# Optimization experiments

Hardware: AMD Instinct MI355X
Metric: run time of the kernel (lower is better)

Reference implementation:

```python
import jax, jax.numpy as jnp
import numpy as np

EPS = 1e-5

def _conv1x1(x, w, b):
    # x: [B, Cin, L], w: [Cout, Cin], b: [Cout]
    return jnp.einsum('oc,bcl->bol', w, x) + b[None, :, None]

def _bn(x, g, b):
    # BatchNorm1d in training mode: batch stats over (B, L), biased variance
    m = jnp.mean(x, axis=(0, 2), keepdims=True)
    v = jnp.var(x, axis=(0, 2), keepdims=True)
    return g[None, :, None] * (x - m) * jax.lax.rsqrt(v + EPS) + b[None, :, None]

def setup_inputs() -> dict:
    key = jax.random.key(0)
    ks = jax.random.split(key, 16)
    B, H, L, K = 32, 32, 32768, 7
    rel, im, out = H // 16, H // 8, H // 4          # 2, 4, 8
    cat = (1 + K) * rel                              # 16
    w = lambda k, shape: jax.random.normal(k, shape, jnp.float32) * 0.1
    return {
        'x': jax.random.normal(ks[0], (B, H, L), jnp.float32),
        'w_phi': w(ks[1], (rel, H)),  'b_phi': w(ks[2], (rel,)),
        'w_psi': w(ks[3], (rel, H)),  'b_psi': w(ks[4], (rel,)),
        'w_beta': w(ks[5], (out, H)), 'b_beta': w(ks[6], (out,)),
        'w_cw1': w(ks[7], (im, cat)), 'b_cw1': w(ks[8], (im,)),
        'w_cw2': w(ks[9], (out, im)), 'b_cw2': w(ks[10], (out,)),
        'w_out': w(ks[11], (H, out)), 'b_out': w(ks[12], (H,)),
        'g_cat': jnp.ones((cat,), jnp.float32),  'be_cat': jnp.zeros((cat,), jnp.float32),
        'g_im': jnp.ones((im,), jnp.float32),    'be_im': jnp.zeros((im,), jnp.float32),
        'g_aggr': jnp.ones((out,), jnp.float32), 'be_aggr': jnp.zeros((out,), jnp.float32),
        'g_hid': jnp.ones((H,), jnp.float32),    'be_hid': jnp.zeros((H,), jnp.float32),
        'kernel_size': 7,
    }

def reference(x, w_phi, b_phi, w_psi, b_psi, w_beta, b_beta,
              w_cw1, b_cw1, w_cw2, b_cw2, w_out, b_out,
              g_cat, be_cat, g_im, be_im, g_aggr, be_aggr, g_hid, be_hid,
              kernel_size):
    B, H, L = x.shape
    phi = _conv1x1(x, w_phi, b_phi)                       # [B, rel, L]
    psi = _conv1x1(x, w_psi, b_psi)                       # [B, rel, L]
    p = kernel_size // 2
    psi_pad = jnp.pad(psi, ((0, 0), (0, 0), (p, p)))
    # F.unfold with kernel (k,1): channel index = c*k + j -> stack kernel axis after channel
    psi_unf = jnp.stack([psi_pad[:, :, j:j + L] for j in range(kernel_size)], axis=2)
    psi_unf = psi_unf.reshape(B, psi.shape[1] * kernel_size, L)   # [B, rel*k, L]
    h = jnp.concatenate([phi, psi_unf], axis=1)           # [B, (1+k)*rel, L]
    h = jax.nn.relu(_bn(h, g_cat, be_cat))
    h = _conv1x1(h, w_cw1, b_cw1)
    h = jax.nn.relu(_bn(h, g_im, be_im))
    weight = _conv1x1(h, w_cw2, b_cw2)                    # [B, out, L]
    beta = _conv1x1(x, w_beta, b_beta)                    # [B, out, L]
    aggr = jax.nn.relu(_bn(weight * beta, g_aggr, be_aggr))
    y = x + _conv1x1(aggr, w_out, b_out)
    return jax.nn.relu(_bn(y, g_hid, be_hid))
```

## Files before the change

### kernel.cpp

```cpp
#include <hip/hip_runtime.h>
#include <math.h>

#define Bn 32
#define Hc 32
#define Ln 32768
#define RELC 2
#define IMC 4
#define OC 8
#define CATC 16
#define KS 7
#define NPOS (Bn*Ln)
#define TPB 256
#define VPT 4
#define PPB (TPB*VPT)
#define TILES (Ln/PPB)
#define NBLK (Bn*TILES)
#define NSLOT 16
#define SSTR 128
#define PCH (RELC*PPB)
#define BCH (OC*PPB)
#define XCH (Hc*PPB)

#define iS_PHI  0
#define iSS_PHI 2
#define iS_PSI  4
#define iSS_PSI 6
#define iS_T    8
#define iSS_T   12
#define iS_AP   16
#define iSS_AP  24
#define iS_Y    32
#define iSS_Y   64
#define bPF  0
#define bPFS 6
#define bQL  12
#define bQLS 18
#define NBST 24

#define FMA4(A,S,V) { A.x=fmaf((S),(V).x,A.x); A.y=fmaf((S),(V).y,A.y); A.z=fmaf((S),(V).z,A.z); A.w=fmaf((S),(V).w,A.w); }

__device__ inline float4 affrelu(float4 v, float a, float d){
    float4 r;
    r.x=fmaxf(fmaf(a,v.x,d),0.f); r.y=fmaxf(fmaf(a,v.y,d),0.f);
    r.z=fmaxf(fmaf(a,v.z,d),0.f); r.w=fmaxf(fmaf(a,v.w,d),0.f);
    return r;
}
__device__ inline double wredd(double v){
    #pragma unroll
    for (int o=32;o>0;o>>=1) v += __shfl_down(v,o,64);
    return v;
}
__device__ inline float wredf(float v){
    #pragma unroll
    for (int o=32;o>0;o>>=1) v += __shfl_down(v,o,64);
    return v;
}
__device__ inline void atomAddD(double* p, double v){ unsafeAtomicAdd(p, v); }

__device__ inline unsigned short f2b(float f){
    unsigned int u = __float_as_uint(f);
    u += 0x7FFFu + ((u>>16)&1u);
    return (unsigned short)(u>>16);
}
__device__ inline float b2f(unsigned short h){ return __uint_as_float(((unsigned int)h)<<16); }
__device__ inline ushort4 pack4r(float4 v, float4* r){
    ushort4 h;
    h.x=f2b(v.x); h.y=f2b(v.y); h.z=f2b(v.z); h.w=f2b(v.w);
    r->x=b2f(h.x); r->y=b2f(h.y); r->z=b2f(h.z); r->w=b2f(h.w);
    return h;
}
__device__ inline ushort4 pack4(float4 v){
    ushort4 h;
    h.x=f2b(v.x); h.y=f2b(v.y); h.z=f2b(v.z); h.w=f2b(v.w);
    return h;
}
__device__ inline float4 unpack4(ushort4 h){
    return make_float4(b2f(h.x),b2f(h.y),b2f(h.z),b2f(h.w));
}
typedef unsigned short us8 __attribute__((ext_vector_type(8)));
typedef float f4nt __attribute__((ext_vector_type(4)));
__device__ inline void ntstore4(float* p, float4 v){
    union { float4 a; f4nt b; } u; u.a = v;
    __builtin_nontemporal_store(u.b, (f4nt*)p);
}

template<int NCH>
__device__ void affines(const double* __restrict__ stats, const double* __restrict__ bstats,
                        const float* g_cat, const float* be_cat,
                        const float* g_im,  const float* be_im,
                        const float* g_ag,  const float* be_ag,
                        const float* g_hid, const float* be_hid,
                        double (*redS)[16], double (*redQ)[16],
                        double* bstL, float* aAll, float* dAll, int tid)
{
    if (tid < NBST) bstL[tid] = bstats[tid];
    for (int p = tid; p < NCH*16; p += TPB){
        int ch = p >> 4, s = p & 15;
        int si, qi;
        if (ch < 2)       { si = iS_PHI+ch;           qi = iSS_PHI+ch; }
        else if (ch < 16) { int cp=(ch-2)/KS;         si = iS_PSI+cp;  qi = iSS_PSI+cp; }
        else if (ch < 20) { int i=ch-16;              si = iS_T+i;     qi = iSS_T+i; }
        else if (ch < 28) { int o=ch-20;              si = iS_AP+o;    qi = iSS_AP+o; }
        else              { int h=ch-28;              si = iS_Y+h;     qi = iSS_Y+h; }
        redS[ch][s] = stats[(size_t)s*SSTR + si];
        redQ[ch][s] = stats[(size_t)s*SSTR + qi];
    }
    __syncthreads();
    if (tid < NCH){
        double S=0, SS=0;
        #pragma unroll
        for (int s=0;s<16;++s){ S += redS[tid][s]; SS += redQ[tid][s]; }
        float g, be;
        if (tid < 16){
            if (tid >= 2){
                int cp=(tid-2)/KS, j=(tid-2)%KS, d=j-KS/2;
                if (d>0) for (int i=0;i<d;++i)   { S-=bstL[bPF+cp*3+i]; SS-=bstL[bPFS+cp*3+i]; }
                if (d<0) for (int i=3+d;i<3;++i) { S-=bstL[bQL+cp*3+i]; SS-=bstL[bQLS+cp*3+i]; }
            }
            g=g_cat[tid]; be=be_cat[tid];
        } else if (tid < 20){ g=g_im[tid-16]; be=be_im[tid-16]; }
        else if (tid < 28){ g=g_ag[tid-20]; be=be_ag[tid-20]; }
        else { g=g_hid[tid-28]; be=be_hid[tid-28]; }
        const double N=(double)NPOS;
        double m=S/N, v=SS/N-m*m, inv=1.0/sqrt(v+1e-5);
        aAll[tid]=(float)(g*inv);
        dAll[tid]=be-(float)(m*inv*g);
    }
}

__global__ void __launch_bounds__(TPB) k0(const float* __restrict__ x, unsigned short* __restrict__ xC)
{
    const int r = blockIdx.x;
    const int b = r >> 5, h = r & 31;
    const float* src = x + (size_t)r*Ln;
    unsigned short* dstBase = xC + (size_t)b*TILES*XCH + (size_t)h*PPB + threadIdx.x*4;
    const float* s4 = src + threadIdx.x*4;
    #pragma unroll 4
    for (int t = 0; t < TILES; ++t){
        float4 v = *(const float4*)(s4 + (size_t)t*PPB);
        *(ushort4*)(dstBase + (size_t)t*XCH) = pack4(v);
    }
}

__global__ void __launch_bounds__(TPB) k1c(
    const unsigned short* __restrict__ xC,
    const float* __restrict__ w_phi, const float* __restrict__ b_phi,
    const float* __restrict__ w_psi, const float* __restrict__ b_psi,
    const float* __restrict__ w_beta,const float* __restrict__ b_beta,
    unsigned short* __restrict__ phiC, unsigned short* __restrict__ psiC,
    unsigned short* __restrict__ betaC,
    double* __restrict__ stats, double* __restrict__ bstats)
{
    __shared__ __align__(16) float wl[Hc*12 + 12];
    __shared__ double rbuf[4][8];
    const int tid = threadIdx.x;
    for (int i = tid; i < Hc*12; i += TPB) {
        int h = i/12, j = i%12;
        float v;
        if (j < 2)      v = w_phi[j*Hc + h];
        else if (j < 4) v = w_psi[(j-2)*Hc + h];
        else            v = w_beta[(j-4)*Hc + h];
        wl[h*12 + j] = v;
    }
    if (tid < 12)
        wl[Hc*12+tid] = (tid<2) ? b_phi[tid] : (tid<4) ? b_psi[tid-2] : b_beta[tid-4];
    __syncthreads();

    const int cidx = blockIdx.x;
    const int tile = cidx % TILES;
    const int li   = tid*VPT;
    double* st = stats + (size_t)(cidx & (NSLOT-1))*SSTR;

    float4 acc[12];
    #pragma unroll
    for (int j=0;j<12;++j){ float bb = wl[Hc*12+j]; acc[j]=make_float4(bb,bb,bb,bb); }

    const unsigned short* xb = xC + (size_t)cidx*XCH + li;
    #pragma unroll
    for (int g=0; g<4; ++g){
        ushort4 xv[8];
        #pragma unroll
        for (int j=0;j<8;++j) xv[j] = *(const ushort4*)(xb + (size_t)(g*8+j)*PPB);
        #pragma unroll
        for (int j=0;j<8;++j){
            const int h = g*8+j;
            const float4 x4 = unpack4(xv[j]);
            const float4 w0 = *(const float4*)(&wl[h*12+0]);
            const float4 w1 = *(const float4*)(&wl[h*12+4]);
            const float4 w2 = *(const float4*)(&wl[h*12+8]);
            FMA4(acc[0],w0.x,x4); FMA4(acc[1],w0.y,x4); FMA4(acc[2],w0.z,x4); FMA4(acc[3],w0.w,x4);
            FMA4(acc[4],w1.x,x4); FMA4(acc[5],w1.y,x4); FMA4(acc[6],w1.z,x4); FMA4(acc[7],w1.w,x4);
            FMA4(acc[8],w2.x,x4); FMA4(acc[9],w2.y,x4); FMA4(acc[10],w2.z,x4); FMA4(acc[11],w2.w,x4);
        }
    }
    float4 rphi[2], rpsi[2];
    #pragma unroll
    for (int c=0;c<RELC;++c){
        ushort4 hp = pack4r(acc[c], &rphi[c]);
        *(ushort4*)(phiC + (size_t)cidx*PCH + c*PPB + li) = hp;
        ushort4 hq = pack4r(acc[2+c], &rpsi[c]);
        *(ushort4*)(psiC + (size_t)cidx*PCH + c*PPB + li) = hq;
    }
    #pragma unroll
    for (int o=0;o<OC;++o)
        *(ushort4*)(betaC + (size_t)cidx*BCH + o*PPB + li) = pack4(acc[4+o]);

    double vals[8];
    #pragma unroll
    for (int c=0;c<2;++c){
        float4 v = rphi[c];
        vals[c]   = (double)v.x+v.y+v.z+v.w;
        vals[2+c] = (double)v.x*v.x+(double)v.y*v.y+(double)v.z*v.z+(double)v.w*v.w;
        float4 u = rpsi[c];
        vals[4+c] = (double)u.x+u.y+u.z+u.w;
        vals[6+c] = (double)u.x*u.x+(double)u.y*u.y+(double)u.z*u.z+(double)u.w*u.w;
    }
    if (tile==0 || tile==TILES-1) {
        #pragma unroll
        for (int c=0;c<2;++c){
            const float pv[4] = {rpsi[c].x, rpsi[c].y, rpsi[c].z, rpsi[c].w};
            #pragma unroll
            for (int e=0;e<4;++e){
                int le = tile*PPB + li + e;
                if (le < 3) {
                    atomAddD(&bstats[bPF +c*3+le], (double)pv[e]);
                    atomAddD(&bstats[bPFS+c*3+le], (double)pv[e]*pv[e]);
                }
                if (le >= Ln-3) {
                    int i = le-(Ln-3);
                    atomAddD(&bstats[bQL +c*3+i], (double)pv[e]);
                    atomAddD(&bstats[bQLS+c*3+i], (double)pv[e]*pv[e]);
                }
            }
        }
    }
    const int lane=tid&63, wid=tid>>6;
    #pragma unroll
    for (int i=0;i<8;++i){ double r=wredd(vals[i]); if(lane==0) rbuf[wid][i]=r; }
    __syncthreads();
    if (tid<8) atomAddD(&st[iS_PHI+tid], rbuf[0][tid]+rbuf[1][tid]+rbuf[2][tid]+rbuf[3][tid]);
}

#define STAGE_PSI_V(psiT)                                                                  \
    {                                                                                      \
        int c_ = tid >> 7, k_ = tid & 127;                                                 \
        us8 v_ = *(const us8*)(psiC + (size_t)cidx*PCH + c_*PPB + 8*k_);                   \
        _Pragma("unroll")                                                                  \
        for (int j_=0;j_<8;++j_) psiT[c_][3+8*k_+j_] = b2f(v_[j_]);                        \
        if (tid < 6){ int cc=tid/3, ii=tid%3;                                              \
            psiT[cc][ii] = (tile>0) ? b2f(psiC[(size_t)(cidx-1)*PCH + cc*PPB + 1021+ii]) : 0.f; }\
        else if (tid < 12){ int kk=tid-6, cc=kk/3, ii=kk%3;                                \
            psiT[cc][1027+ii] = (tile<TILES-1) ? b2f(psiC[(size_t)(cidx+1)*PCH + cc*PPB + ii]) : 0.f; } \
    }

#define COMPUTE_T(tacc,aCat,dCat,w1s,b1s,psiT)                                             \
    _Pragma("unroll")                                                                      \
    for (int o=0;o<IMC;++o){ float bb=b1s[o]; tacc[o]=make_float4(bb,bb,bb,bb); }          \
    _Pragma("unroll")                                                                      \
    for (int c=0;c<RELC;++c){                                                              \
        float4 pv = unpack4(*(const ushort4*)(phiC + (size_t)cidx*PCH + c*PPB + li));      \
        float4 hv = affrelu(pv, aCat[c], dCat[c]);                                         \
        _Pragma("unroll")                                                                  \
        for (int o=0;o<IMC;++o) FMA4(tacc[o], w1s[o*CATC+c], hv);                          \
    }                                                                                      \
    _Pragma("unroll")                                                                      \
    for (int c=0;c<RELC;++c){                                                              \
        float4 A  = *(const float4*)&psiT[c][li];                                          \
        float4 Bv = *(const float4*)&psiT[c][li+4];                                        \
        float4 Cv = *(const float4*)&psiT[c][li+8];                                        \
        float pr[12] = {A.x,A.y,A.z,A.w, Bv.x,Bv.y,Bv.z,Bv.w, Cv.x,Cv.y,Cv.z,Cv.w};        \
        _Pragma("unroll")                                                                  \
        for (int j=0;j<KS;++j){                                                            \
            int ch = 2 + c*KS + j;                                                         \
            float a=aCat[ch], d=dCat[ch];                                                  \
            float4 hv;                                                                     \
            hv.x=fmaxf(fmaf(a,pr[j+0],d),0.f);                                             \
            hv.y=fmaxf(fmaf(a,pr[j+1],d),0.f);                                             \
            hv.z=fmaxf(fmaf(a,pr[j+2],d),0.f);                                             \
            hv.w=fmaxf(fmaf(a,pr[j+3],d),0.f);                                             \
            _Pragma("unroll")                                                              \
            for (int o=0;o<IMC;++o) FMA4(tacc[o], w1s[o*CATC+ch], hv);                     \
        }                                                                                  \
    }

#define COMPUTE_AG(ag,tacc,aIm,dIm,aAg,dAg,w2s,b2s)                                        \
    {                                                                                      \
        float4 h2[IMC];                                                                    \
        _Pragma("unroll")                                                                  \
        for (int i=0;i<IMC;++i) h2[i]=affrelu(tacc[i],aIm[i],dIm[i]);                      \
        _Pragma("unroll")                                                                  \
        for (int o=0;o<OC;++o){                                                            \
            float bb=b2s[o];                                                               \
            float4 w=make_float4(bb,bb,bb,bb);                                             \
            _Pragma("unroll")                                                              \
            for (int i=0;i<IMC;++i) FMA4(w,w2s[o*IMC+i],h2[i]);                            \
            float4 bv = unpack4(*(const ushort4*)(betaC + (size_t)cidx*BCH + o*PPB + li)); \
            float4 av; av.x=w.x*bv.x; av.y=w.y*bv.y; av.z=w.z*bv.z; av.w=w.w*bv.w;         \
            ag[o]=affrelu(av, aAg[o], dAg[o]);                                             \
        }                                                                                  \
    }

__global__ void __launch_bounds__(TPB) k3t(
    const unsigned short* __restrict__ phiC, const unsigned short* __restrict__ psiC,
    const float* __restrict__ w_cw1, const float* __restrict__ b_cw1,
    const float* __restrict__ g_cat, const float* __restrict__ be_cat,
    double* __restrict__ stats, const double* __restrict__ bstats)
{
    __shared__ float w1s[IMC*CATC], b1s[IMC];
    __shared__ __align__(16) float psiT[2][1032];
    __shared__ double rbuf[4][8];
    __shared__ double redS[16][16], redQ[16][16];
    __shared__ double bstL[NBST];
    __shared__ float aAll[16], dAll[16];
    const int tid = threadIdx.x;
    const int cidx = blockIdx.x;
    const int tile = cidx % TILES;
    const int li   = tid*VPT;
    double* st = stats + (size_t)(cidx & (NSLOT-1))*SSTR;

    if (tid < IMC*CATC) w1s[tid] = w_cw1[tid];
    if (tid < IMC)      b1s[tid] = b_cw1[tid];
    STAGE_PSI_V(psiT)
    affines<16>(stats,bstats, g_cat,be_cat, 0,0, 0,0, 0,0, redS,redQ,bstL,aAll,dAll, tid);
    __syncthreads();

    float4 tacc[IMC];
    COMPUTE_T(tacc,aAll,dAll,w1s,b1s,psiT)

    double vals[8];
    #pragma unroll
    for (int o=0;o<IMC;++o){
        float4 v = tacc[o];
        vals[o]   = (double)v.x+v.y+v.z+v.w;
        vals[4+o] = (double)v.x*v.x+(double)v.y*v.y+(double)v.z*v.z+(double)v.w*v.w;
    }
    const int lane=tid&63, wid=tid>>6;
    #pragma unroll
    for (int i=0;i<8;++i){ double r=wredd(vals[i]); if(lane==0) rbuf[wid][i]=r; }
    __syncthreads();
    if (tid<8) atomAddD(&st[iS_T+tid], rbuf[0][tid]+rbuf[1][tid]+rbuf[2][tid]+rbuf[3][tid]);
}

__global__ void __launch_bounds__(TPB) k5a(
    const unsigned short* __restrict__ phiC, const unsigned short* __restrict__ psiC,
    const unsigned short* __restrict__ betaC,
    const float* __restrict__ w_cw1, const float* __restrict__ b_cw1,
    const float* __restrict__ w_cw2, const float* __restrict__ b_cw2,
    const float* __restrict__ g_cat, const float* __restrict__ be_cat,
    const float* __restrict__ g_im,  const float* __restrict__ be_im,
    double* __restrict__ stats, const double* __restrict__ bstats)
{
    __shared__ float w1s[IMC*CATC], b1s[IMC], w2s[OC*IMC], b2s[OC];
    __shared__ __align__(16) float psiT[2][1032];
    __shared__ double rbuf[4][16];
    __shared__ double redS[20][16], redQ[20][16];
    __shared__ double bstL[NBST];
    __shared__ float aAll[20], dAll[20];
    const int tid = threadIdx.x;
    const int cidx = blockIdx.x;
    const int tile = cidx % TILES;
    const int li   = tid*VPT;
    double* st = stats + (size_t)(cidx & (NSLOT-1))*SSTR;

    if (tid < IMC*CATC) w1s[tid] = w_cw1[tid];
    if (tid < IMC)      b1s[tid] = b_cw1[tid];
    if (tid>=64 && tid<64+OC*IMC) w2s[tid-64]=w_cw2[tid-64];
    if (tid>=96 && tid<96+OC)     b2s[tid-96]=b_cw2[tid-96];
    STAGE_PSI_V(psiT)
    affines<20>(stats,bstats, g_cat,be_cat, g_im,be_im, 0,0, 0,0, redS,redQ,bstL,aAll,dAll, tid);
    __syncthreads();

    float4 tacc[IMC];
    COMPUTE_T(tacc,aAll,dAll,w1s,b1s,psiT)

    double vals[16];
    {
        float4 h2[IMC];
        #pragma unroll
        for (int i=0;i<IMC;++i) h2[i]=affrelu(tacc[i],aAll[16+i],dAll[16+i]);
        #pragma unroll
        for (int o=0;o<OC;++o){
            float bb=b2s[o];
            float4 w=make_float4(bb,bb,bb,bb);
            #pragma unroll
            for (int i=0;i<IMC;++i) FMA4(w,w2s[o*IMC+i],h2[i]);
            float4 bv = unpack4(*(const ushort4*)(betaC + (size_t)cidx*BCH + o*PPB + li));
            float4 av; av.x=w.x*bv.x; av.y=w.y*bv.y; av.z=w.z*bv.z; av.w=w.w*bv.w;
            vals[o]   = (double)av.x+av.y+av.z+av.w;
            vals[8+o] = (double)av.x*av.x+(double)av.y*av.y+(double)av.z*av.z+(double)av.w*av.w;
        }
    }
    const int lane=tid&63, wid=tid>>6;
    #pragma unroll
    for (int i=0;i<16;++i){ double r=wredd(vals[i]); if(lane==0) rbuf[wid][i]=r; }
    __syncthreads();
    if (tid<16) atomAddD(&st[iS_AP+tid], rbuf[0][tid]+rbuf[1][tid]+rbuf[2][tid]+rbuf[3][tid]);
}

__global__ void __launch_bounds__(TPB) k7y(
    const unsigned short* __restrict__ xC,
    const unsigned short* __restrict__ phiC, const unsigned short* __restrict__ psiC,
    const unsigned short* __restrict__ betaC, unsigned short* __restrict__ agC,
    const float* __restrict__ w_cw1, const float* __restrict__ b_cw1,
    const float* __restrict__ w_cw2, const float* __restrict__ b_cw2,
    const float* __restrict__ w_out, const float* __restrict__ b_out,
    const float* __restrict__ g_cat, const float* __restrict__ be_cat,
    const float* __restrict__ g_im,  const float* __restrict__ be_im,
    const float* __restrict__ g_ag,  const float* __restrict__ be_ag,
    double* __restrict__ stats, const double* __restrict__ bstats)
{
    __shared__ float w1s[IMC*CATC], b1s[IMC], w2s[OC*IMC], b2s[OC];
    __shared__ __align__(16) float wos[Hc*OC];
    __shared__ float bos[Hc];
    __shared__ __align__(16) float psiT[2][1032];
    __shared__ float fredS[Hc][4], fredQ[Hc][4];
    __shared__ double redS[28][16], redQ[28][16];
    __shared__ double bstL[NBST];
    __shared__ float aAll[28], dAll[28];
    const int tid = threadIdx.x;
    const int cidx = blockIdx.x;
    const int tile = cidx % TILES;
    const int li   = tid*VPT;
    double* st = stats + (size_t)(cidx & (NSLOT-1))*SSTR;

    if (tid < IMC*CATC) w1s[tid] = w_cw1[tid];
    if (tid < IMC)      b1s[tid] = b_cw1[tid];
    if (tid>=64 && tid<64+OC*IMC) w2s[tid-64]=w_cw2[tid-64];
    if (tid>=96 && tid<96+OC)     b2s[tid-96]=b_cw2[tid-96];
    wos[tid] = w_out[tid];
    if (tid>=128 && tid<128+Hc) bos[tid-128]=b_out[tid-128];
    STAGE_PSI_V(psiT)
    affines<28>(stats,bstats, g_cat,be_cat, g_im,be_im, g_ag,be_ag, 0,0,
                redS,redQ,bstL,aAll,dAll, tid);
    __syncthreads();

    float4 tacc[IMC];
    COMPUTE_T(tacc,aAll,dAll,w1s,b1s,psiT)
    float4 ag[OC];
    COMPUTE_AG(ag,tacc,(aAll+16),(dAll+16),(aAll+20),(dAll+20),w2s,b2s)
    #pragma unroll
    for (int o=0;o<OC;++o){
        ushort4 hh = pack4r(ag[o], &ag[o]);
        *(ushort4*)(agC + (size_t)cidx*BCH + o*PPB + li) = hh;
    }

    const int lane=tid&63, wid=tid>>6;
    const unsigned short* xb = xC + (size_t)cidx*XCH + li;
    #pragma unroll
    for (int g=0; g<4; ++g){
        ushort4 xv[8];
        #pragma unroll
        for (int j=0;j<8;++j) xv[j] = *(const ushort4*)(xb + (size_t)(g*8+j)*PPB);
        #pragma unroll
        for (int j=0;j<8;++j){
            const int h = g*8+j;
            float4 y = unpack4(xv[j]);
            float bb=bos[h]; y.x+=bb; y.y+=bb; y.z+=bb; y.w+=bb;
            #pragma unroll
            for (int o=0;o<OC;++o) FMA4(y, wos[h*OC+o], ag[o]);
            float fs=y.x+y.y+y.z+y.w;
            float fq=y.x*y.x+y.y*y.y+y.z*y.z+y.w*y.w;
            fs=wredf(fs); fq=wredf(fq);
            if (lane==0){ fredS[h][wid]=fs; fredQ[h][wid]=fq; }
        }
    }
    __syncthreads();
    if (tid<Hc){
        double s=(double)fredS[tid][0]+fredS[tid][1]+fredS[tid][2]+fredS[tid][3];
        double q=(double)fredQ[tid][0]+fredQ[tid][1]+fredQ[tid][2]+fredQ[tid][3];
        atomAddD(&st[iS_Y +tid], s);
        atomAddD(&st[iSS_Y+tid], q);
    }
}

__global__ void __launch_bounds__(TPB) k9s(
    const unsigned short* __restrict__ xC, const unsigned short* __restrict__ agC,
    const float* __restrict__ w_out, const float* __restrict__ b_out,
    const float* __restrict__ g_hid, const float* __restrict__ be_hid,
    float* __restrict__ out, const double* __restrict__ stats)
{
    __shared__ double redS[Hc][16], redQ[Hc][16];
    __shared__ float aH[Hc], dH[Hc];
    __shared__ __align__(16) float wos[Hc*OC];
    __shared__ float bos[Hc];
    const int tid = threadIdx.x;
    const int cidx = blockIdx.x;
    const int b    = cidx / TILES;
    const int tile = cidx % TILES;
    const int li   = tid*VPT;

    wos[tid] = w_out[tid];
    if (tid>=128 && tid<128+Hc) bos[tid-128]=b_out[tid-128];
    for (int p = tid; p < Hc*16; p += TPB){
        int ch = p >> 4, s = p & 15;
        redS[ch][s] = stats[(size_t)s*SSTR + iS_Y + ch];
        redQ[ch][s] = stats[(size_t)s*SSTR + iSS_Y + ch];
    }
    __syncthreads();
    if (tid < Hc){
        double S=0, SS=0;
        #pragma unroll
        for (int s=0;s<16;++s){ S += redS[tid][s]; SS += redQ[tid][s]; }
        const double N=(double)NPOS;
        double m=S/N, v=SS/N-m*m, inv=1.0/sqrt(v+1e-5);
        aH[tid]=(float)(g_hid[tid]*inv);
        dH[tid]=be_hid[tid]-(float)(m*inv*g_hid[tid]);
    }
    __syncthreads();

    float4 ag[OC];
    {
        ushort4 av[OC];
        #pragma unroll
        for (int o=0;o<OC;++o) av[o] = *(const ushort4*)(agC + (size_t)cidx*BCH + o*PPB + li);
        #pragma unroll
        for (int o=0;o<OC;++o) ag[o] = unpack4(av[o]);
    }
    const unsigned short* xb = xC + (size_t)cidx*XCH + li;
    float* ob = out + (size_t)b*Hc*Ln + (size_t)tile*PPB + li;
    #pragma unroll
    for (int g=0; g<4; ++g){
        ushort4 xv[8];
        #pragma unroll
        for (int j=0;j<8;++j) xv[j] = *(const ushort4*)(xb + (size_t)(g*8+j)*PPB);
        #pragma unroll
        for (int j=0;j<8;++j){
            const int h = g*8+j;
            float4 y = unpack4(xv[j]);
            float bb=bos[h]; y.x+=bb; y.y+=bb; y.z+=bb; y.w+=bb;
            #pragma unroll
            for (int o=0;o<OC;++o) FMA4(y, wos[h*OC+o], ag[o]);
            ntstore4(ob + (size_t)h*Ln, affrelu(y, aH[h], dH[h]));
        }
    }
}

extern "C" void kernel_launch(void* const* d_in, const int* in_sizes, int n_in,
                              void* d_out, int out_size, void* d_ws, size_t ws_size,
                              hipStream_t stream)
{
    const float* x     =(const float*)d_in[0];
    const float* w_phi =(const float*)d_in[1];  const float* b_phi =(const float*)d_in[2];
    const float* w_psi =(const float*)d_in[3];  const float* b_psi =(const float*)d_in[4];
    const float* w_beta=(const float*)d_in[5];  const float* b_beta=(const float*)d_in[6];
    const float* w_cw1 =(const float*)d_in[7];  const float* b_cw1 =(const float*)d_in[8];
    const float* w_cw2 =(const float*)d_in[9];  const float* b_cw2 =(const float*)d_in[10];
    const float* w_out =(const float*)d_in[11]; const float* b_out =(const float*)d_in[12];
    const float* g_cat =(const float*)d_in[13]; const float* be_cat=(const float*)d_in[14];
    const float* g_im  =(const float*)d_in[15]; const float* be_im =(const float*)d_in[16];
    const float* g_ag  =(const float*)d_in[17]; const float* be_ag =(const float*)d_in[18];
    const float* g_hid =(const float*)d_in[19]; const float* be_hid=(const float*)d_in[20];

    double* stats  = (double*)d_ws;
    double* bstats = stats + (size_t)NSLOT*SSTR;
    unsigned short* base = (unsigned short*)((char*)d_ws + 32768);
    unsigned short* phiC  = base;
    unsigned short* psiC  = phiC  + (size_t)NBLK*PCH;
    unsigned short* betaC = psiC  + (size_t)NBLK*PCH;
    unsigned short* xC    = betaC + (size_t)NBLK*BCH;
    unsigned short* agC   = xC    + (size_t)NBLK*XCH;

    hipMemsetAsync(d_ws, 0, ((size_t)NSLOT*SSTR + NBST)*sizeof(double), stream);
    k0 <<<Bn*Hc, TPB, 0, stream>>>(x, xC);
    k1c<<<NBLK, TPB, 0, stream>>>(xC, w_phi,b_phi, w_psi,b_psi, w_beta,b_beta,
                                  phiC,psiC,betaC, stats,bstats);
    k3t<<<NBLK, TPB, 0, stream>>>(phiC,psiC, w_cw1,b_cw1, g_cat,be_cat, stats,bstats);
    k5a<<<NBLK, TPB, 0, stream>>>(phiC,psiC,betaC, w_cw1,b_cw1, w_cw2,b_cw2,
                                  g_cat,be_cat, g_im,be_im, stats,bstats);
    k7y<<<NBLK, TPB, 0, stream>>>(xC, phiC,psiC,betaC, agC, w_cw1,b_cw1, w_cw2,b_cw2,
                                  w_out,b_out, g_cat,be_cat, g_im,be_im, g_ag,be_ag,
                                  stats,bstats);
    k9s<<<NBLK, TPB, 0, stream>>>(xC, agC, w_out,b_out, g_hid,be_hid,
                                  (float*)d_out, stats);
}
```

Baseline: 166.9 us.

## Fold stats zeroing into k0, split k0 rows, halve k3t grid

Removes the separate memset launch by having block 0 of k0 zero the statistics buffers. k0 now runs twice as many blocks, each converting half of a row, to improve parallelism. k3t processes two tiles per block, so it recomputes the BN affines and does the stat atomics only half as often. Block 0 zeroing stats inside k0 is ordered before k1c only by stream ordering, which holds.

```diff
diff --git a/kernel.cpp b/kernel.cpp
--- a/kernel.cpp
+++ b/kernel.cpp
@@ -36,6 +36,7 @@
 #define bQL  12
 #define bQLS 18
 #define NBST 24
+#define NZERO ((size_t)NSLOT*SSTR + NBST)
 
 #define FMA4(A,S,V) { A.x=fmaf((S),(V).x,A.x); A.y=fmaf((S),(V).y,A.y); A.z=fmaf((S),(V).z,A.z); A.w=fmaf((S),(V).w,A.w); }
 
@@ -128,15 +129,22 @@
     }
 }
 
-__global__ void __launch_bounds__(TPB) k0(const float* __restrict__ x, unsigned short* __restrict__ xC)
-{
-    const int r = blockIdx.x;
+__global__ void __launch_bounds__(TPB) k0(const float* __restrict__ x, unsigned short* __restrict__ xC,
+                                          double* __restrict__ statz)
+{
+    if (blockIdx.x == 0){
+        for (size_t i = threadIdx.x; i < NZERO; i += TPB) statz[i] = 0.0;
+    }
+    const int rr = blockIdx.x;
+    const int r  = rr >> 1;
+    const int half = rr & 1;
     const int b = r >> 5, h = r & 31;
-    const float* src = x + (size_t)r*Ln;
-    unsigned short* dstBase = xC + (size_t)b*TILES*XCH + (size_t)h*PPB + threadIdx.x*4;
+    const float* src = x + (size_t)r*Ln + (size_t)half*(Ln/2);
+    unsigned short* dstBase = xC + (size_t)b*TILES*XCH + (size_t)(half*(TILES/2))*XCH
+                               + (size_t)h*PPB + threadIdx.x*4;
     const float* s4 = src + threadIdx.x*4;
     #pragma unroll 4
-    for (int t = 0; t < TILES; ++t){
+    for (int t = 0; t < TILES/2; ++t){
         float4 v = *(const float4*)(s4 + (size_t)t*PPB);
         *(ushort4*)(dstBase + (size_t)t*XCH) = pack4(v);
     }
@@ -313,31 +321,34 @@
     __shared__ double bstL[NBST];
     __shared__ float aAll[16], dAll[16];
     const int tid = threadIdx.x;
-    const int cidx = blockIdx.x;
-    const int tile = cidx % TILES;
     const int li   = tid*VPT;
-    double* st = stats + (size_t)(cidx & (NSLOT-1))*SSTR;
 
     if (tid < IMC*CATC) w1s[tid] = w_cw1[tid];
     if (tid < IMC)      b1s[tid] = b_cw1[tid];
-    STAGE_PSI_V(psiT)
     affines<16>(stats,bstats, g_cat,be_cat, 0,0, 0,0, 0,0, redS,redQ,bstL,aAll,dAll, tid);
-    __syncthreads();
-
-    float4 tacc[IMC];
-    COMPUTE_T(tacc,aAll,dAll,w1s,b1s,psiT)
-
-    double vals[8];
-    #pragma unroll
-    for (int o=0;o<IMC;++o){
-        float4 v = tacc[o];
-        vals[o]   = (double)v.x+v.y+v.z+v.w;
-        vals[4+o] = (double)v.x*v.x+(double)v.y*v.y+(double)v.z*v.z+(double)v.w*v.w;
+
+    double vals[8] = {0,0,0,0,0,0,0,0};
+    for (int sub=0; sub<2; ++sub){
+        const int cidx = blockIdx.x*2 + sub;
+        const int tile = cidx % TILES;
+        __syncthreads();
+        STAGE_PSI_V(psiT)
+        __syncthreads();
+
+        float4 tacc[IMC];
+        COMPUTE_T(tacc,aAll,dAll,w1s,b1s,psiT)
+        #pragma unroll
+        for (int o=0;o<IMC;++o){
+            float4 v = tacc[o];
+            vals[o]   += (double)v.x+v.y+v.z+v.w;
+            vals[4+o] += (double)v.x*v.x+(double)v.y*v.y+(double)v.z*v.z+(double)v.w*v.w;
+        }
     }
     const int lane=tid&63, wid=tid>>6;
     #pragma unroll
     for (int i=0;i<8;++i){ double r=wredd(vals[i]); if(lane==0) rbuf[wid][i]=r; }
     __syncthreads();
+    double* st = stats + (size_t)(blockIdx.x & (NSLOT-1))*SSTR;
     if (tid<8) atomAddD(&st[iS_T+tid], rbuf[0][tid]+rbuf[1][tid]+rbuf[2][tid]+rbuf[3][tid]);
 }
 
@@ -560,11 +571,10 @@
     unsigned short* xC    = betaC + (size_t)NBLK*BCH;
     unsigned short* agC   = xC    + (size_t)NBLK*XCH;
 
-    hipMemsetAsync(d_ws, 0, ((size_t)NSLOT*SSTR + NBST)*sizeof(double), stream);
-    k0 <<<Bn*Hc, TPB, 0, stream>>>(x, xC);
+    k0 <<<Bn*Hc*2, TPB, 0, stream>>>(x, xC, stats);
     k1c<<<NBLK, TPB, 0, stream>>>(xC, w_phi,b_phi, w_psi,b_psi, w_beta,b_beta,
                                   phiC,psiC,betaC, stats,bstats);
-    k3t<<<NBLK, TPB, 0, stream>>>(phiC,psiC, w_cw1,b_cw1, g_cat,be_cat, stats,bstats);
+    k3t<<<NBLK/2, TPB, 0, stream>>>(phiC,psiC, w_cw1,b_cw1, g_cat,be_cat, stats,bstats);
     k5a<<<NBLK, TPB, 0, stream>>>(phiC,psiC,betaC, w_cw1,b_cw1, w_cw2,b_cw2,
                                   g_cat,be_cat, g_im,be_im, stats,bstats);
     k7y<<<NBLK, TPB, 0, stream>>>(xC, phiC,psiC,betaC, agC, w_cw1,b_cw1, w_cw2,b_cw2,
```

New measurement: 157.8 us. 1.06x faster.
